# Kernel optimization log

Hardware: AMD Instinct MI355X
Metric: run time of the kernel (lower is better)

Reference implementation:

```python
import jax, jax.numpy as jnp
import numpy as np

D = 1024      # hidden_size
F = 4096      # intermediate_size
E = 16        # num_experts
TOPK = 2      # num_experts_per_tok
B, L = 1, 2048


def setup_inputs() -> dict:
    key = jax.random.key(0)
    ks = jax.random.split(key, 5)
    s = 0.02
    return {
        "x": jax.random.normal(ks[0], (B, L, D), dtype=jnp.float32),
        "gate_w": jax.random.normal(ks[1], (E, D), dtype=jnp.float32) * s,
        "w1s": jax.random.normal(ks[2], (E, F, D), dtype=jnp.float32) * s,  # per-expert w1 (out,in)
        "w2s": jax.random.normal(ks[3], (E, D, F), dtype=jnp.float32) * s,  # per-expert w2
        "w3s": jax.random.normal(ks[4], (E, F, D), dtype=jnp.float32) * s,  # per-expert w3
    }


def reference(x, gate_w, w1s, w2s, w3s):
    b, l, d = x.shape
    xf = x.reshape(-1, d)                                   # [T, D]
    router_logits = xf @ gate_w.T                           # [T, E]
    topw, topi = jax.lax.top_k(router_logits.astype(jnp.float32), TOPK)
    topw = jax.nn.softmax(topw, axis=-1).astype(x.dtype)    # [T, K]
    T = xf.shape[0]
    # dense combine weights: zero for unselected experts (same math as masked loop)
    combine = jnp.zeros((T, E), x.dtype).at[jnp.arange(T)[:, None], topi].add(topw)

    def body(acc, ew):
        w1, w2, w3, cw = ew                                 # cw: [T]
        h = jax.nn.silu(xf @ w1.T) * (xf @ w3.T)            # [T, F]
        return acc + cw[:, None] * (h @ w2.T), None

    out, _ = jax.lax.scan(body, jnp.zeros_like(xf), (w1s, w2s, w3s, combine.T))
    return out.reshape(b, l, d), router_logits
```

## Files before the change

### kernel.cpp

```cpp
#include <hip/hip_runtime.h>

#define D_DIM 1024
#define F_DIM 4096
#define E_NUM 16
#define T_NUM 2048

typedef __bf16 bf16x8 __attribute__((ext_vector_type(8)));
typedef float f32x4 __attribute__((ext_vector_type(4)));

__device__ __forceinline__ unsigned pack2bf(float a, float b) {
  unsigned ua = __builtin_bit_cast(unsigned, a);
  unsigned ub = __builtin_bit_cast(unsigned, b);
  return ((ub + 0x8000u) & 0xffff0000u) | ((ua + 0x8000u) >> 16);
}
__device__ __forceinline__ unsigned short f2bf(float a) {
  unsigned ua = __builtin_bit_cast(unsigned, a);
  return (unsigned short)((ua + 0x8000u) >> 16);
}
__device__ __forceinline__ bf16x8 cvt8(f32x4 a, f32x4 b) {
  bf16x8 r;
  r[0] = (__bf16)a[0]; r[1] = (__bf16)a[1]; r[2] = (__bf16)a[2]; r[3] = (__bf16)a[3];
  r[4] = (__bf16)b[0]; r[5] = (__bf16)b[1]; r[6] = (__bf16)b[2]; r[7] = (__bf16)b[3];
  return r;
}
__device__ __forceinline__ void gload16(const void* g, void* l) {
  __builtin_amdgcn_global_load_lds(
      (const __attribute__((address_space(1))) unsigned*)g,
      (__attribute__((address_space(3))) unsigned*)l, 16, 0, 0);
}

__global__ __launch_bounds__(256) void moe_xcast(
    const float* __restrict__ x, unsigned short* __restrict__ xbf)
{
  int i = blockIdx.x * 256 + threadIdx.x;
  const f32x4* p = (const f32x4*)x + (size_t)i * 2;
  f32x4 a = p[0], b = p[1];
  uint4 o;
  o.x = pack2bf(a[0], a[1]); o.y = pack2bf(a[2], a[3]);
  o.z = pack2bf(b[0], b[1]); o.w = pack2bf(b[2], b[3]);
  ((uint4*)xbf)[i] = o;
}

__global__ __launch_bounds__(256) void moe_router(
    const float* __restrict__ x, const float* __restrict__ gate,
    float* __restrict__ logits_out, int* __restrict__ topi, float* __restrict__ topw)
{
  __shared__ float lg[16][17];
  int tid = threadIdx.x;
  int tbase = blockIdx.x * 16;
  int tt = tid >> 4, e = tid & 15;
  const float4* xr = (const float4*)(x + (size_t)(tbase + tt) * D_DIM);
  const float4* gw = (const float4*)(gate + (size_t)e * D_DIM);
  float acc = 0.f;
  #pragma unroll 4
  for (int k = 0; k < D_DIM / 4; ++k) {
    float4 a = xr[k], b = gw[k];
    acc += a.x * b.x + a.y * b.y + a.z * b.z + a.w * b.w;
  }
  lg[tt][e] = acc;
  logits_out[(size_t)(tbase + tt) * E_NUM + e] = acc;
  __syncthreads();
  if (tid < 16) {
    int t = tid;
    float best = -1e30f; int i0 = 0;
    #pragma unroll
    for (int j = 0; j < 16; ++j) { float v = lg[t][j]; if (v > best) { best = v; i0 = j; } }
    float best1 = -1e30f; int i1 = 0;
    #pragma unroll
    for (int j = 0; j < 16; ++j) { if (j == i0) continue; float v = lg[t][j]; if (v > best1) { best1 = v; i1 = j; } }
    float e1 = __expf(best1 - best);
    float inv = 1.f / (1.f + e1);
    int gt = tbase + t;
    topi[gt * 2]     = i0;  topi[gt * 2 + 1] = i1;
    topw[gt * 2]     = inv; topw[gt * 2 + 1] = e1 * inv;
  }
}

__global__ __launch_bounds__(1024) void moe_route_build(
    const int* __restrict__ topi,
    int* __restrict__ cnt, int* __restrict__ rowbase,
    int* __restrict__ rowlist, int* __restrict__ rowpos)
{
  __shared__ int scnt[16];
  __shared__ int sbase[17];
  int wave = threadIdx.x >> 6;
  int lane = threadIdx.x & 63;
  int total = 0;
  for (int c = 0; c < (T_NUM * 2) / 64; ++c) {
    int s = c * 64 + lane;
    unsigned long long m = __ballot(topi[s] == wave);
    total += __popcll(m);
  }
  if (lane == 0) scnt[wave] = total;
  __syncthreads();
  if (threadIdx.x == 0) {
    int acc = 0;
    for (int e2 = 0; e2 < 16; ++e2) { sbase[e2] = acc; cnt[e2] = scnt[e2]; acc += scnt[e2]; }
    sbase[16] = acc;
    for (int e2 = 0; e2 <= 16; ++e2) rowbase[e2] = sbase[e2];
  }
  __syncthreads();
  int running = sbase[wave];
  for (int c = 0; c < (T_NUM * 2) / 64; ++c) {
    int s = c * 64 + lane;
    int ei = topi[s];
    unsigned long long m = __ballot(ei == wave);
    if (ei == wave) {
      int pos = running + __popcll(m & ((1ull << lane) - 1ull));
      rowlist[pos] = s;
      rowpos[s] = pos;
    }
    running += __popcll(m);
  }
}

__global__ __launch_bounds__(512, 2) void moe_gemm1(
    const unsigned short* __restrict__ xbf, const float* __restrict__ w1s, const float* __restrict__ w3s,
    const int* __restrict__ cnt, const int* __restrict__ rowbase, const int* __restrict__ rowlist,
    unsigned short* __restrict__ H)
{
  int bid = blockIdx.x;
  int xcd = bid & 7, j = bid >> 3;
  int e = xcd * 2 + (j >> 5);
  int nt = j & 31;
  int Ne = cnt[e];
  int rbase = rowbase[e];
  int nmt = (Ne + 255) >> 8;

  __shared__ char smem[98304];

  int tid = threadIdx.x, lane = tid & 63, wave = tid >> 6;

  const float* w1e = w1s + (size_t)e * F_DIM * D_DIM + (size_t)(nt * 128) * D_DIM;
  const float* w3e = w3s + (size_t)e * F_DIM * D_DIM + (size_t)(nt * 128) * D_DIM;
  const char* p1[2]; const char* p3[2];
  #pragma unroll
  for (int it = 0; it < 2; ++it) {
    int r = (wave * 2 + it) * 8 + (lane >> 3);
    int c = (lane & 7) ^ (r & 7);
    p1[it] = (const char*)(w1e + (size_t)r * D_DIM) + c * 16;
    p3[it] = (const char*)(w3e + (size_t)r * D_DIM) + c * 16;
  }

  int xrr[2]; int xc[2];
  #pragma unroll
  for (int it = 0; it < 2; ++it) {
    xrr[it] = (wave * 2 + it) * 16 + (lane >> 2);
    xc[it] = (lane & 3) ^ ((xrr[it] >> 1) & 3);
  }

  int wm = wave >> 1, wn = wave & 1;
  int lr16 = lane & 15, lq = lane >> 4;

  unsigned offA[4];
  #pragma unroll
  for (int mi = 0; mi < 4; ++mi) {
    int m = wm * 64 + mi * 16 + lr16;
    offA[mi] = (unsigned)(m * 64 + ((lq ^ ((m >> 1) & 3)) * 16));
  }
  unsigned offB[4][2];
  #pragma unroll
  for (int ni = 0; ni < 4; ++ni) {
    int n = wn * 64 + ni * 16 + lr16;
    #pragma unroll
    for (int h = 0; h < 2; ++h)
      offB[ni][h] = (unsigned)(n * 128 + (((lq * 2 + h) ^ (n & 7)) * 16));
  }

  unsigned xdst = (unsigned)((wave * 2) * 1024 + lane * 16);
  unsigned wdst = (unsigned)((wave * 2) * 1024 + lane * 16);

  for (int mt = 0; mt < nmt; ++mt) {
    const char* px[2];
    #pragma unroll
    for (int it = 0; it < 2; ++it) {
      int xlr = mt * 256 + xrr[it];
      int tok = (xlr < Ne) ? (rowlist[rbase + xlr] >> 1) : 0;
      px[it] = (const char*)(xbf + (size_t)tok * D_DIM) + xc[it] * 16;
    }

    f32x4 acc1[4][4], acc3[4][4];
    #pragma unroll
    for (int i = 0; i < 4; ++i)
      #pragma unroll
      for (int jj = 0; jj < 4; ++jj) { acc1[i][jj] = {0.f,0.f,0.f,0.f}; acc3[i][jj] = {0.f,0.f,0.f,0.f}; }

    auto STAGE = [&](unsigned bsel, int ks) {
      gload16(px[0] + ks * 64, smem + bsel * 16384 + xdst);
      gload16(px[1] + ks * 64, smem + bsel * 16384 + xdst + 1024);
      #pragma unroll
      for (int it = 0; it < 2; ++it) {
        gload16(p1[it] + ks * 128, smem + 32768 + bsel * 16384 + wdst + it * 1024);
        gload16(p3[it] + ks * 128, smem + 65536 + bsel * 16384 + wdst + it * 1024);
      }
    };

    STAGE(0, 0);
    unsigned buf = 0;
    for (int ks = 0; ks < 32; ++ks) {
      if (ks < 31) {
        STAGE(buf ^ 1u, ks + 1);
        asm volatile("s_waitcnt vmcnt(6)" ::: "memory");
      } else {
        asm volatile("s_waitcnt vmcnt(0)" ::: "memory");
      }
      __builtin_amdgcn_s_barrier();
      unsigned xb = buf * 16384;
      unsigned w1b = 32768 + buf * 16384;
      unsigned w3b = 65536 + buf * 16384;
      bf16x8 af[4];
      #pragma unroll
      for (int mi = 0; mi < 4; ++mi)
        af[mi] = *(const bf16x8*)(smem + xb + offA[mi]);
      #pragma unroll
      for (int ni = 0; ni < 4; ++ni) {
        bf16x8 b1 = cvt8(*(const f32x4*)(smem + w1b + offB[ni][0]),
                         *(const f32x4*)(smem + w1b + offB[ni][1]));
        bf16x8 b3 = cvt8(*(const f32x4*)(smem + w3b + offB[ni][0]),
                         *(const f32x4*)(smem + w3b + offB[ni][1]));
        #pragma unroll
        for (int mi = 0; mi < 4; ++mi) {
          acc1[mi][ni] = __builtin_amdgcn_mfma_f32_16x16x32_bf16(af[mi], b1, acc1[mi][ni], 0, 0, 0);
          acc3[mi][ni] = __builtin_amdgcn_mfma_f32_16x16x32_bf16(af[mi], b3, acc3[mi][ni], 0, 0, 0);
        }
      }
      __builtin_amdgcn_s_barrier();
      buf ^= 1u;
    }

    #pragma unroll
    for (int mi = 0; mi < 4; ++mi) {
      int mb = wm * 64 + mi * 16 + lq * 4;
      #pragma unroll
      for (int r = 0; r < 4; ++r) {
        int lrow = mt * 256 + mb + r;
        if (lrow < Ne) {
          size_t hrow = (size_t)(rbase + lrow) * F_DIM;
          #pragma unroll
          for (int ni = 0; ni < 4; ++ni) {
            int f = nt * 128 + wn * 64 + ni * 16 + lr16;
            float a1v = acc1[mi][ni][r];
            float a3v = acc3[mi][ni][r];
            float hv = (a1v / (1.f + __expf(-a1v))) * a3v;
            H[hrow + f] = f2bf(hv);
          }
        }
      }
    }
  }
}

__global__ __launch_bounds__(512, 2) void moe_gemm2(
    const unsigned short* __restrict__ H, const float* __restrict__ w2s,
    const int* __restrict__ cnt, const int* __restrict__ rowbase,
    unsigned short* __restrict__ Ybf)
{
  int bid = blockIdx.x;
  int xcd = bid & 7, j = bid >> 3;
  int e = xcd * 2 + (j >> 4);
  int nt = j & 15;
  int Ne = cnt[e];
  int rbase = rowbase[e];
  int nmt = (Ne + 255) >> 8;

  __shared__ char smem[98304];

  int tid = threadIdx.x, lane = tid & 63, wave = tid >> 6;

  const float* w2e = w2s + (size_t)e * D_DIM * F_DIM + (size_t)(nt * 64) * F_DIM;
  const char* pb[2];
  #pragma unroll
  for (int it = 0; it < 2; ++it) {
    int r = (wave * 2 + it) * 4 + (lane >> 4);
    int c = (lane & 15) ^ (r & 7);
    pb[it] = (const char*)(w2e + (size_t)r * F_DIM) + c * 16;
  }

  int arr[4]; int ac[4];
  #pragma unroll
  for (int it = 0; it < 4; ++it) {
    arr[it] = (wave * 4 + it) * 8 + (lane >> 3);
    ac[it] = (lane & 7) ^ (arr[it] & 7);
  }

  int wm = wave >> 1, wn = wave & 1;
  int lr16 = lane & 15, lq = lane >> 4;

  unsigned dst2 = (unsigned)((wave * 2) * 1024 + lane * 16);
  unsigned dst4 = (unsigned)((wave * 4) * 1024 + lane * 16);

  for (int mt = 0; mt < nmt; ++mt) {
    const char* pa[4];
    #pragma unroll
    for (int it = 0; it < 4; ++it) {
      int grow = mt * 256 + arr[it]; if (grow >= Ne) grow = Ne - 1;
      pa[it] = (const char*)(H + (size_t)(rbase + grow) * F_DIM) + ac[it] * 16;
    }

    f32x4 acc[4][2];
    #pragma unroll
    for (int i = 0; i < 4; ++i) { acc[i][0] = {0.f,0.f,0.f,0.f}; acc[i][1] = {0.f,0.f,0.f,0.f}; }

    auto STAGE = [&](unsigned bsel, int ks) {
      #pragma unroll
      for (int it = 0; it < 4; ++it)
        gload16(pa[it] + ks * 128, smem + bsel * 32768 + dst4 + it * 1024);
      #pragma unroll
      for (int it = 0; it < 2; ++it)
        gload16(pb[it] + ks * 256, smem + 65536 + bsel * 16384 + dst2 + it * 1024);
    };

    STAGE(0, 0);
    unsigned buf = 0;
    for (int ks = 0; ks < 64; ++ks) {
      if (ks < 63) {
        STAGE(buf ^ 1u, ks + 1);
        asm volatile("s_waitcnt vmcnt(6)" ::: "memory");
      } else {
        asm volatile("s_waitcnt vmcnt(0)" ::: "memory");
      }
      __builtin_amdgcn_s_barrier();
      unsigned ab = buf * 32768;
      unsigned bb = 65536 + buf * 16384;
      #pragma unroll
      for (int ksub = 0; ksub < 2; ++ksub) {
        bf16x8 bfr[2];
        #pragma unroll
        for (int ni = 0; ni < 2; ++ni) {
          int n = wn * 32 + ni * 16 + lr16;
          unsigned o0 = (unsigned)(n * 256 + (((ksub * 8 + lq * 2 + 0) ^ (n & 7)) * 16));
          unsigned o1 = (unsigned)(n * 256 + (((ksub * 8 + lq * 2 + 1) ^ (n & 7)) * 16));
          bfr[ni] = cvt8(*(const f32x4*)(smem + bb + o0), *(const f32x4*)(smem + bb + o1));
        }
        #pragma unroll
        for (int mi = 0; mi < 4; ++mi) {
          int m = wm * 64 + mi * 16 + lr16;
          unsigned off = (unsigned)(m * 128 + (((ksub * 4 + lq) ^ (m & 7)) * 16));
          bf16x8 af = *(const bf16x8*)(smem + ab + off);
          #pragma unroll
          for (int ni = 0; ni < 2; ++ni)
            acc[mi][ni] = __builtin_amdgcn_mfma_f32_16x16x32_bf16(af, bfr[ni], acc[mi][ni], 0, 0, 0);
        }
      }
      __builtin_amdgcn_s_barrier();
      buf ^= 1u;
    }

    #pragma unroll
    for (int mi = 0; mi < 4; ++mi) {
      int mb = wm * 64 + mi * 16 + lq * 4;
      #pragma unroll
      for (int r = 0; r < 4; ++r) {
        int lrow = mt * 256 + mb + r;
        if (lrow < Ne) {
          size_t yrow = (size_t)(rbase + lrow) * D_DIM;
          #pragma unroll
          for (int ni = 0; ni < 2; ++ni) {
            int d = nt * 64 + wn * 32 + ni * 16 + lr16;
            Ybf[yrow + d] = f2bf(acc[mi][ni][r]);
          }
        }
      }
    }
  }
}

__global__ __launch_bounds__(128) void moe_combine(
    const unsigned short* __restrict__ Ybf, const int* __restrict__ rowpos,
    const float* __restrict__ topw, float* __restrict__ out)
{
  int t = blockIdx.x, tid = threadIdx.x;
  int r0 = rowpos[t * 2], r1 = rowpos[t * 2 + 1];
  float p0 = topw[t * 2], p1 = topw[t * 2 + 1];
  uint4 a = ((const uint4*)(Ybf + (size_t)r0 * D_DIM))[tid];
  uint4 b = ((const uint4*)(Ybf + (size_t)r1 * D_DIM))[tid];
  float4 o0, o1;
  #define LO(u) __builtin_bit_cast(float, (unsigned)((u) << 16))
  #define HI(u) __builtin_bit_cast(float, (unsigned)((u) & 0xffff0000u))
  o0.x = p0 * LO(a.x) + p1 * LO(b.x);  o0.y = p0 * HI(a.x) + p1 * HI(b.x);
  o0.z = p0 * LO(a.y) + p1 * LO(b.y);  o0.w = p0 * HI(a.y) + p1 * HI(b.y);
  o1.x = p0 * LO(a.z) + p1 * LO(b.z);  o1.y = p0 * HI(a.z) + p1 * HI(b.z);
  o1.z = p0 * LO(a.w) + p1 * LO(b.w);  o1.w = p0 * HI(a.w) + p1 * HI(b.w);
  #undef LO
  #undef HI
  float4* orow = (float4*)(out + (size_t)t * D_DIM);
  orow[tid * 2]     = o0;
  orow[tid * 2 + 1] = o1;
}

extern "C" void kernel_launch(void* const* d_in, const int* in_sizes, int n_in,
                              void* d_out, int out_size, void* d_ws, size_t ws_size,
                              hipStream_t stream) {
  const float* x    = (const float*)d_in[0];
  const float* gate = (const float*)d_in[1];
  const float* w1   = (const float*)d_in[2];
  const float* w2   = (const float*)d_in[3];
  const float* w3   = (const float*)d_in[4];
  float* out    = (float*)d_out;
  float* logits = out + (size_t)T_NUM * D_DIM;

  char* ws = (char*)d_ws;
  int*   cnt     = (int*)(ws + 0);
  int*   rowbase = (int*)(ws + 64);
  int*   topi    = (int*)(ws + 1024);
  float* topw    = (float*)(ws + 1024 + 16384);
  int*   rowlist = (int*)(ws + 1024 + 32768);
  int*   rowpos  = (int*)(ws + 1024 + 49152);
  unsigned short* H   = (unsigned short*)(ws + 131072);
  unsigned short* Ybf = (unsigned short*)(ws + 131072 + 33554432);
  unsigned short* xbf = (unsigned short*)(ws + 131072 + 33554432 + 8388608);

  moe_xcast<<<(T_NUM * D_DIM) / (256 * 8), 256, 0, stream>>>(x, xbf);
  moe_router<<<T_NUM / 16, 256, 0, stream>>>(x, gate, logits, topi, topw);
  moe_route_build<<<1, 1024, 0, stream>>>(topi, cnt, rowbase, rowlist, rowpos);
  moe_gemm1<<<512, 512, 0, stream>>>(xbf, w1, w3, cnt, rowbase, rowlist, H);
  moe_gemm2<<<256, 512, 0, stream>>>(H, w2, cnt, rowbase, Ybf);
  moe_combine<<<T_NUM, 128, 0, stream>>>(Ybf, rowpos, topw, out);
}
```

Before: 381.4 us.

## Triple-buffer LDS staging with prefetch distance two in both MoE GEMMs

Both expert GEMM kernels move from double-buffered to triple-buffered shared-memory staging. Tile loads are now issued two k-steps ahead, and the vmcnt waits are adjusted so more global loads stay in flight during the MFMA work. The goal is to hide global memory latency better on the fp32 weight streams. The cost is a larger LDS footprint, rising from 96KB to 144KB per block.

```diff
diff --git a/kernel.cpp b/kernel.cpp
--- a/kernel.cpp
+++ b/kernel.cpp
@@ -127,7 +127,7 @@
   int rbase = rowbase[e];
   int nmt = (Ne + 255) >> 8;
 
-  __shared__ char smem[98304];
+  __shared__ char smem[147456];
 
   int tid = threadIdx.x, lane = tid & 63, wave = tid >> 6;
 
@@ -186,38 +186,41 @@
       for (int jj = 0; jj < 4; ++jj) { acc1[i][jj] = {0.f,0.f,0.f,0.f}; acc3[i][jj] = {0.f,0.f,0.f,0.f}; }
 
     auto STAGE = [&](unsigned bsel, int ks) {
-      gload16(px[0] + ks * 64, smem + bsel * 16384 + xdst);
-      gload16(px[1] + ks * 64, smem + bsel * 16384 + xdst + 1024);
+      unsigned bo = bsel * 16384u;
+      gload16(px[0] + ks * 64, smem + bo + xdst);
+      gload16(px[1] + ks * 64, smem + bo + xdst + 1024);
       #pragma unroll
       for (int it = 0; it < 2; ++it) {
-        gload16(p1[it] + ks * 128, smem + 32768 + bsel * 16384 + wdst + it * 1024);
-        gload16(p3[it] + ks * 128, smem + 65536 + bsel * 16384 + wdst + it * 1024);
+        gload16(p1[it] + ks * 128, smem + 49152 + bo + wdst + it * 1024);
+        gload16(p3[it] + ks * 128, smem + 98304 + bo + wdst + it * 1024);
       }
     };
 
     STAGE(0, 0);
-    unsigned buf = 0;
+    STAGE(1, 1);
+    unsigned cb = 0;
     for (int ks = 0; ks < 32; ++ks) {
-      if (ks < 31) {
-        STAGE(buf ^ 1u, ks + 1);
+      if (ks < 30) {
+        unsigned sb = (cb == 0) ? 2u : cb - 1u;
+        STAGE(sb, ks + 2);
+        asm volatile("s_waitcnt vmcnt(12)" ::: "memory");
+      } else if (ks == 30) {
         asm volatile("s_waitcnt vmcnt(6)" ::: "memory");
       } else {
         asm volatile("s_waitcnt vmcnt(0)" ::: "memory");
       }
       __builtin_amdgcn_s_barrier();
-      unsigned xb = buf * 16384;
-      unsigned w1b = 32768 + buf * 16384;
-      unsigned w3b = 65536 + buf * 16384;
+      unsigned bo = cb * 16384u;
       bf16x8 af[4];
       #pragma unroll
       for (int mi = 0; mi < 4; ++mi)
-        af[mi] = *(const bf16x8*)(smem + xb + offA[mi]);
+        af[mi] = *(const bf16x8*)(smem + bo + offA[mi]);
       #pragma unroll
       for (int ni = 0; ni < 4; ++ni) {
-        bf16x8 b1 = cvt8(*(const f32x4*)(smem + w1b + offB[ni][0]),
-                         *(const f32x4*)(smem + w1b + offB[ni][1]));
-        bf16x8 b3 = cvt8(*(const f32x4*)(smem + w3b + offB[ni][0]),
-                         *(const f32x4*)(smem + w3b + offB[ni][1]));
+        bf16x8 b1 = cvt8(*(const f32x4*)(smem + 49152 + bo + offB[ni][0]),
+                         *(const f32x4*)(smem + 49152 + bo + offB[ni][1]));
+        bf16x8 b3 = cvt8(*(const f32x4*)(smem + 98304 + bo + offB[ni][0]),
+                         *(const f32x4*)(smem + 98304 + bo + offB[ni][1]));
         #pragma unroll
         for (int mi = 0; mi < 4; ++mi) {
           acc1[mi][ni] = __builtin_amdgcn_mfma_f32_16x16x32_bf16(af[mi], b1, acc1[mi][ni], 0, 0, 0);
@@ -225,7 +228,7 @@
         }
       }
       __builtin_amdgcn_s_barrier();
-      buf ^= 1u;
+      cb = (cb == 2) ? 0u : cb + 1u;
     }
 
     #pragma unroll
@@ -263,7 +266,7 @@
   int rbase = rowbase[e];
   int nmt = (Ne + 255) >> 8;
 
-  __shared__ char smem[98304];
+  __shared__ char smem[147456];
 
   int tid = threadIdx.x, lane = tid & 63, wave = tid >> 6;
 
@@ -304,24 +307,28 @@
     auto STAGE = [&](unsigned bsel, int ks) {
       #pragma unroll
       for (int it = 0; it < 4; ++it)
-        gload16(pa[it] + ks * 128, smem + bsel * 32768 + dst4 + it * 1024);
+        gload16(pa[it] + ks * 128, smem + bsel * 32768u + dst4 + it * 1024);
       #pragma unroll
       for (int it = 0; it < 2; ++it)
-        gload16(pb[it] + ks * 256, smem + 65536 + bsel * 16384 + dst2 + it * 1024);
+        gload16(pb[it] + ks * 256, smem + 98304 + bsel * 16384u + dst2 + it * 1024);
     };
 
     STAGE(0, 0);
-    unsigned buf = 0;
+    STAGE(1, 1);
+    unsigned cb = 0;
     for (int ks = 0; ks < 64; ++ks) {
-      if (ks < 63) {
-        STAGE(buf ^ 1u, ks + 1);
+      if (ks < 62) {
+        unsigned sb = (cb == 0) ? 2u : cb - 1u;
+        STAGE(sb, ks + 2);
+        asm volatile("s_waitcnt vmcnt(12)" ::: "memory");
+      } else if (ks == 62) {
         asm volatile("s_waitcnt vmcnt(6)" ::: "memory");
       } else {
         asm volatile("s_waitcnt vmcnt(0)" ::: "memory");
       }
       __builtin_amdgcn_s_barrier();
-      unsigned ab = buf * 32768;
-      unsigned bb = 65536 + buf * 16384;
+      unsigned ab = cb * 32768u;
+      unsigned bb = 98304 + cb * 16384u;
       #pragma unroll
       for (int ksub = 0; ksub < 2; ++ksub) {
         bf16x8 bfr[2];
@@ -343,7 +350,7 @@
         }
       }
       __builtin_amdgcn_s_barrier();
-      buf ^= 1u;
+      cb = (cb == 2) ? 0u : cb + 1u;
     }
 
     #pragma unroll
```

After: 392.4 us. 1.03x slower.

## Split MoE GEMMs over M-tiles in a 3D grid with 320-row tiles

Applied to the files above, without the earlier changes.

Both expert GEMM kernels drop their in-block loop over 256-row M tiles. Each block now handles one 320-row tile, launched over a (N-tile, M-tile, expert) grid, and blocks past the expert's row count exit early. This spreads imbalanced expert loads across more blocks and uses larger M tiles for more weight reuse per loaded tile. In exchange it uses more LDS and accumulator registers per block, which may lower occupancy, drops the XCD-aware expert mapping, and reloads weights once per M tile.

```diff
diff --git a/kernel.cpp b/kernel.cpp
--- a/kernel.cpp
+++ b/kernel.cpp
@@ -119,15 +119,12 @@
     const int* __restrict__ cnt, const int* __restrict__ rowbase, const int* __restrict__ rowlist,
     unsigned short* __restrict__ H)
 {
-  int bid = blockIdx.x;
-  int xcd = bid & 7, j = bid >> 3;
-  int e = xcd * 2 + (j >> 5);
-  int nt = j & 31;
+  int nt = blockIdx.x, mt = blockIdx.y, e = blockIdx.z;
   int Ne = cnt[e];
+  if (mt * 320 >= Ne) return;
   int rbase = rowbase[e];
-  int nmt = (Ne + 255) >> 8;
-
-  __shared__ char smem[98304];
+
+  __shared__ char smem[107520];
 
   int tid = threadIdx.x, lane = tid & 63, wave = tid >> 6;
 
@@ -142,20 +139,31 @@
     p3[it] = (const char*)(w3e + (size_t)r * D_DIM) + c * 16;
   }
 
-  int xrr[2]; int xc[2];
-  #pragma unroll
-  for (int it = 0; it < 2; ++it) {
-    xrr[it] = (wave * 2 + it) * 16 + (lane >> 2);
-    xc[it] = (lane & 3) ^ ((xrr[it] >> 1) & 3);
+  const char* px[3];
+  unsigned xdoff[3];
+  #pragma unroll
+  for (int it = 0; it < 3; ++it) {
+    int ch = wave + it * 8;
+    if (ch < 20) {
+      int r = ch * 16 + (lane >> 2);
+      int lr = mt * 320 + r;
+      int tok = (lr < Ne) ? (rowlist[rbase + lr] >> 1) : 0;
+      int c = (lane & 3) ^ ((r >> 1) & 3);
+      px[it] = (const char*)(xbf + (size_t)tok * D_DIM) + c * 16;
+      xdoff[it] = (unsigned)(ch * 1024 + lane * 16);
+    } else {
+      px[it] = (const char*)xbf + (lane & 3) * 16;
+      xdoff[it] = 0xFFFFFFFFu;
+    }
   }
 
   int wm = wave >> 1, wn = wave & 1;
   int lr16 = lane & 15, lq = lane >> 4;
 
-  unsigned offA[4];
-  #pragma unroll
-  for (int mi = 0; mi < 4; ++mi) {
-    int m = wm * 64 + mi * 16 + lr16;
+  unsigned offA[5];
+  #pragma unroll
+  for (int mi = 0; mi < 5; ++mi) {
+    int m = wm * 80 + mi * 16 + lr16;
     offA[mi] = (unsigned)(m * 64 + ((lq ^ ((m >> 1) & 3)) * 16));
   }
   unsigned offB[4][2];
@@ -167,83 +175,77 @@
       offB[ni][h] = (unsigned)(n * 128 + (((lq * 2 + h) ^ (n & 7)) * 16));
   }
 
-  unsigned xdst = (unsigned)((wave * 2) * 1024 + lane * 16);
   unsigned wdst = (unsigned)((wave * 2) * 1024 + lane * 16);
 
-  for (int mt = 0; mt < nmt; ++mt) {
-    const char* px[2];
+  f32x4 acc1[5][4], acc3[5][4];
+  #pragma unroll
+  for (int i = 0; i < 5; ++i)
+    #pragma unroll
+    for (int j = 0; j < 4; ++j) { acc1[i][j] = {0.f,0.f,0.f,0.f}; acc3[i][j] = {0.f,0.f,0.f,0.f}; }
+
+  auto STAGE = [&](unsigned bsel, int ks) {
+    #pragma unroll
+    for (int it = 0; it < 3; ++it) {
+      char* dst = (xdoff[it] == 0xFFFFFFFFu)
+                    ? (smem + 106496 + lane * 16)
+                    : (smem + bsel * 20480u + xdoff[it]);
+      gload16(px[it] + ks * 64, dst);
+    }
     #pragma unroll
     for (int it = 0; it < 2; ++it) {
-      int xlr = mt * 256 + xrr[it];
-      int tok = (xlr < Ne) ? (rowlist[rbase + xlr] >> 1) : 0;
-      px[it] = (const char*)(xbf + (size_t)tok * D_DIM) + xc[it] * 16;
-    }
-
-    f32x4 acc1[4][4], acc3[4][4];
-    #pragma unroll
-    for (int i = 0; i < 4; ++i)
+      gload16(p1[it] + ks * 128, smem + 40960 + bsel * 16384u + wdst + it * 1024);
+      gload16(p3[it] + ks * 128, smem + 73728 + bsel * 16384u + wdst + it * 1024);
+    }
+  };
+
+  STAGE(0, 0);
+  unsigned buf = 0;
+  for (int ks = 0; ks < 32; ++ks) {
+    if (ks < 31) {
+      STAGE(buf ^ 1u, ks + 1);
+      asm volatile("s_waitcnt vmcnt(7)" ::: "memory");
+    } else {
+      asm volatile("s_waitcnt vmcnt(0)" ::: "memory");
+    }
+    __builtin_amdgcn_s_barrier();
+    unsigned xb = buf * 20480u;
+    unsigned w1b = 40960 + buf * 16384u;
+    unsigned w3b = 73728 + buf * 16384u;
+    bf16x8 af[5];
+    #pragma unroll
+    for (int mi = 0; mi < 5; ++mi)
+      af[mi] = *(const bf16x8*)(smem + xb + offA[mi]);
+    #pragma unroll
+    for (int ni = 0; ni < 4; ++ni) {
+      bf16x8 b1 = cvt8(*(const f32x4*)(smem + w1b + offB[ni][0]),
+                       *(const f32x4*)(smem + w1b + offB[ni][1]));
+      bf16x8 b3 = cvt8(*(const f32x4*)(smem + w3b + offB[ni][0]),
+                       *(const f32x4*)(smem + w3b + offB[ni][1]));
       #pragma unroll
-      for (int jj = 0; jj < 4; ++jj) { acc1[i][jj] = {0.f,0.f,0.f,0.f}; acc3[i][jj] = {0.f,0.f,0.f,0.f}; }
-
-    auto STAGE = [&](unsigned bsel, int ks) {
-      gload16(px[0] + ks * 64, smem + bsel * 16384 + xdst);
-      gload16(px[1] + ks * 64, smem + bsel * 16384 + xdst + 1024);
-      #pragma unroll
-      for (int it = 0; it < 2; ++it) {
-        gload16(p1[it] + ks * 128, smem + 32768 + bsel * 16384 + wdst + it * 1024);
-        gload16(p3[it] + ks * 128, smem + 65536 + bsel * 16384 + wdst + it * 1024);
+      for (int mi = 0; mi < 5; ++mi) {
+        acc1[mi][ni] = __builtin_amdgcn_mfma_f32_16x16x32_bf16(af[mi], b1, acc1[mi][ni], 0, 0, 0);
+        acc3[mi][ni] = __builtin_amdgcn_mfma_f32_16x16x32_bf16(af[mi], b3, acc3[mi][ni], 0, 0, 0);
       }
-    };
-
-    STAGE(0, 0);
-    unsigned buf = 0;
-    for (int ks = 0; ks < 32; ++ks) {
-      if (ks < 31) {
-        STAGE(buf ^ 1u, ks + 1);
-        asm volatile("s_waitcnt vmcnt(6)" ::: "memory");
-      } else {
-        asm volatile("s_waitcnt vmcnt(0)" ::: "memory");
-      }
-      __builtin_amdgcn_s_barrier();
-      unsigned xb = buf * 16384;
-      unsigned w1b = 32768 + buf * 16384;
-      unsigned w3b = 65536 + buf * 16384;
-      bf16x8 af[4];
-      #pragma unroll
-      for (int mi = 0; mi < 4; ++mi)
-        af[mi] = *(const bf16x8*)(smem + xb + offA[mi]);
-      #pragma unroll
-      for (int ni = 0; ni < 4; ++ni) {
-        bf16x8 b1 = cvt8(*(const f32x4*)(smem + w1b + offB[ni][0]),
-                         *(const f32x4*)(smem + w1b + offB[ni][1]));
-        bf16x8 b3 = cvt8(*(const f32x4*)(smem + w3b + offB[ni][0]),
-                         *(const f32x4*)(smem + w3b + offB[ni][1]));
+    }
+    __builtin_amdgcn_s_barrier();
+    buf ^= 1u;
+  }
+
+  #pragma unroll
+  for (int mi = 0; mi < 5; ++mi) {
+    int mb = wm * 80 + mi * 16 + lq * 4;
+    #pragma unroll
+    for (int r = 0; r < 4; ++r) {
+      int lrow = mt * 320 + mb + r;
+      if (lrow < Ne) {
+        size_t hrow = (size_t)(rbase + lrow) * F_DIM;
         #pragma unroll
-        for (int mi = 0; mi < 4; ++mi) {
-          acc1[mi][ni] = __builtin_amdgcn_mfma_f32_16x16x32_bf16(af[mi], b1, acc1[mi][ni], 0, 0, 0);
-          acc3[mi][ni] = __builtin_amdgcn_mfma_f32_16x16x32_bf16(af[mi], b3, acc3[mi][ni], 0, 0, 0);
-        }
-      }
-      __builtin_amdgcn_s_barrier();
-      buf ^= 1u;
-    }
-
-    #pragma unroll
-    for (int mi = 0; mi < 4; ++mi) {
-      int mb = wm * 64 + mi * 16 + lq * 4;
-      #pragma unroll
-      for (int r = 0; r < 4; ++r) {
-        int lrow = mt * 256 + mb + r;
-        if (lrow < Ne) {
-          size_t hrow = (size_t)(rbase + lrow) * F_DIM;
-          #pragma unroll
-          for (int ni = 0; ni < 4; ++ni) {
-            int f = nt * 128 + wn * 64 + ni * 16 + lr16;
-            float a1v = acc1[mi][ni][r];
-            float a3v = acc3[mi][ni][r];
-            float hv = (a1v / (1.f + __expf(-a1v))) * a3v;
-            H[hrow + f] = f2bf(hv);
-          }
+        for (int ni = 0; ni < 4; ++ni) {
+          int f = nt * 128 + wn * 64 + ni * 16 + lr16;
+          float a1v = acc1[mi][ni][r];
+          float a3v = acc3[mi][ni][r];
+          float hv = (a1v / (1.f + __expf(-a1v))) * a3v;
+          H[hrow + f] = f2bf(hv);
         }
       }
     }
@@ -255,15 +257,12 @@
     const int* __restrict__ cnt, const int* __restrict__ rowbase,
     unsigned short* __restrict__ Ybf)
 {
-  int bid = blockIdx.x;
-  int xcd = bid & 7, j = bid >> 3;
-  int e = xcd * 2 + (j >> 4);
-  int nt = j & 15;
+  int nt = blockIdx.x, mt = blockIdx.y, e = blockIdx.z;
   int Ne = cnt[e];
+  if (mt * 320 >= Ne) return;
   int rbase = rowbase[e];
-  int nmt = (Ne + 255) >> 8;
-
-  __shared__ char smem[98304];
+
+  __shared__ char smem[114688];
 
   int tid = threadIdx.x, lane = tid & 63, wave = tid >> 6;
 
@@ -276,89 +275,84 @@
     pb[it] = (const char*)(w2e + (size_t)r * F_DIM) + c * 16;
   }
 
-  int arr[4]; int ac[4];
-  #pragma unroll
-  for (int it = 0; it < 4; ++it) {
-    arr[it] = (wave * 4 + it) * 8 + (lane >> 3);
-    ac[it] = (lane & 7) ^ (arr[it] & 7);
+  const char* pa[5];
+  unsigned adoff[5];
+  #pragma unroll
+  for (int it = 0; it < 5; ++it) {
+    int ch = wave + it * 8;
+    int r = ch * 8 + (lane >> 3);
+    int grow = mt * 320 + r; if (grow >= Ne) grow = Ne - 1;
+    int c = (lane & 7) ^ (r & 7);
+    pa[it] = (const char*)(H + (size_t)(rbase + grow) * F_DIM) + c * 16;
+    adoff[it] = (unsigned)(ch * 1024 + lane * 16);
   }
 
   int wm = wave >> 1, wn = wave & 1;
   int lr16 = lane & 15, lq = lane >> 4;
 
-  unsigned dst2 = (unsigned)((wave * 2) * 1024 + lane * 16);
-  unsigned dst4 = (unsigned)((wave * 4) * 1024 + lane * 16);
-
-  for (int mt = 0; mt < nmt; ++mt) {
-    const char* pa[4];
-    #pragma unroll
-    for (int it = 0; it < 4; ++it) {
-      int grow = mt * 256 + arr[it]; if (grow >= Ne) grow = Ne - 1;
-      pa[it] = (const char*)(H + (size_t)(rbase + grow) * F_DIM) + ac[it] * 16;
-    }
-
-    f32x4 acc[4][2];
-    #pragma unroll
-    for (int i = 0; i < 4; ++i) { acc[i][0] = {0.f,0.f,0.f,0.f}; acc[i][1] = {0.f,0.f,0.f,0.f}; }
-
-    auto STAGE = [&](unsigned bsel, int ks) {
+  unsigned dstB = (unsigned)((wave * 2) * 1024 + lane * 16);
+
+  f32x4 acc[5][2];
+  #pragma unroll
+  for (int i = 0; i < 5; ++i) { acc[i][0] = {0.f,0.f,0.f,0.f}; acc[i][1] = {0.f,0.f,0.f,0.f}; }
+
+  auto STAGE = [&](unsigned bsel, int ks) {
+    #pragma unroll
+    for (int it = 0; it < 5; ++it)
+      gload16(pa[it] + ks * 128, smem + bsel * 40960u + adoff[it]);
+    #pragma unroll
+    for (int it = 0; it < 2; ++it)
+      gload16(pb[it] + ks * 256, smem + 81920 + bsel * 16384u + dstB + it * 1024);
+  };
+
+  STAGE(0, 0);
+  unsigned buf = 0;
+  for (int ks = 0; ks < 64; ++ks) {
+    if (ks < 63) {
+      STAGE(buf ^ 1u, ks + 1);
+      asm volatile("s_waitcnt vmcnt(7)" ::: "memory");
+    } else {
+      asm volatile("s_waitcnt vmcnt(0)" ::: "memory");
+    }
+    __builtin_amdgcn_s_barrier();
+    unsigned ab = buf * 40960u;
+    unsigned bb = 81920 + buf * 16384u;
+    #pragma unroll
+    for (int ksub = 0; ksub < 2; ++ksub) {
+      bf16x8 bfr[2];
       #pragma unroll
-      for (int it = 0; it < 4; ++it)
-        gload16(pa[it] + ks * 128, smem + bsel * 32768 + dst4 + it * 1024);
+      for (int ni = 0; ni < 2; ++ni) {
+        int n = wn * 32 + ni * 16 + lr16;
+        unsigned o0 = (unsigned)(n * 256 + (((ksub * 8 + lq * 2 + 0) ^ (n & 7)) * 16));
+        unsigned o1 = (unsigned)(n * 256 + (((ksub * 8 + lq * 2 + 1) ^ (n & 7)) * 16));
+        bfr[ni] = cvt8(*(const f32x4*)(smem + bb + o0), *(const f32x4*)(smem + bb + o1));
+      }
       #pragma unroll
-      for (int it = 0; it < 2; ++it)
-        gload16(pb[it] + ks * 256, smem + 65536 + bsel * 16384 + dst2 + it * 1024);
-    };
-
-    STAGE(0, 0);
-    unsigned buf = 0;
-    for (int ks = 0; ks < 64; ++ks) {
-      if (ks < 63) {
-        STAGE(buf ^ 1u, ks + 1);
-        asm volatile("s_waitcnt vmcnt(6)" ::: "memory");
-      } else {
-        asm volatile("s_waitcnt vmcnt(0)" ::: "memory");
+      for (int mi = 0; mi < 5; ++mi) {
+        int m = wm * 80 + mi * 16 + lr16;
+        unsigned off = (unsigned)(m * 128 + (((ksub * 4 + lq) ^ (m & 7)) * 16));
+        bf16x8 af = *(const bf16x8*)(smem + ab + off);
+        #pragma unroll
+        for (int ni = 0; ni < 2; ++ni)
+          acc[mi][ni] = __builtin_amdgcn_mfma_f32_16x16x32_bf16(af, bfr[ni], acc[mi][ni], 0, 0, 0);
       }
-      __builtin_amdgcn_s_barrier();
-      unsigned ab = buf * 32768;
-      unsigned bb = 65536 + buf * 16384;
-      #pragma unroll
-      for (int ksub = 0; ksub < 2; ++ksub) {
-        bf16x8 bfr[2];
+    }
+    __builtin_amdgcn_s_barrier();
+    buf ^= 1u;
+  }
+
+  #pragma unroll
+  for (int mi = 0; mi < 5; ++mi) {
+    int mb = wm * 80 + mi * 16 + lq * 4;
+    #pragma unroll
+    for (int r = 0; r < 4; ++r) {
+      int lrow = mt * 320 + mb + r;
+      if (lrow < Ne) {
+        size_t yrow = (size_t)(rbase + lrow) * D_DIM;
         #pragma unroll
         for (int ni = 0; ni < 2; ++ni) {
-          int n = wn * 32 + ni * 16 + lr16;
-          unsigned o0 = (unsigned)(n * 256 + (((ksub * 8 + lq * 2 + 0) ^ (n & 7)) * 16));
-          unsigned o1 = (unsigned)(n * 256 + (((ksub * 8 + lq * 2 + 1) ^ (n & 7)) * 16));
-          bfr[ni] = cvt8(*(const f32x4*)(smem + bb + o0), *(const f32x4*)(smem + bb + o1));
-        }
-        #pragma unroll
-        for (int mi = 0; mi < 4; ++mi) {
-          int m = wm * 64 + mi * 16 + lr16;
-          unsigned off = (unsigned)(m * 128 + (((ksub * 4 + lq) ^ (m & 7)) * 16));
-          bf16x8 af = *(const bf16x8*)(smem + ab + off);
-          #pragma unroll
-          for (int ni = 0; ni < 2; ++ni)
-            acc[mi][ni] = __builtin_amdgcn_mfma_f32_16x16x32_bf16(af, bfr[ni], acc[mi][ni], 0, 0, 0);
-        }
-      }
-      __builtin_amdgcn_s_barrier();
-      buf ^= 1u;
-    }
-
-    #pragma unroll
-    for (int mi = 0; mi < 4; ++mi) {
-      int mb = wm * 64 + mi * 16 + lq * 4;
-      #pragma unroll
-      for (int r = 0; r < 4; ++r) {
-        int lrow = mt * 256 + mb + r;
-        if (lrow < Ne) {
-          size_t yrow = (size_t)(rbase + lrow) * D_DIM;
-          #pragma unroll
-          for (int ni = 0; ni < 2; ++ni) {
-            int d = nt * 64 + wn * 32 + ni * 16 + lr16;
-            Ybf[yrow + d] = f2bf(acc[mi][ni][r]);
-          }
+          int d = nt * 64 + wn * 32 + ni * 16 + lr16;
+          Ybf[yrow + d] = f2bf(acc[mi][ni][r]);
         }
       }
     }
@@ -413,7 +407,7 @@
   moe_xcast<<<(T_NUM * D_DIM) / (256 * 8), 256, 0, stream>>>(x, xbf);
   moe_router<<<T_NUM / 16, 256, 0, stream>>>(x, gate, logits, topi, topw);
   moe_route_build<<<1, 1024, 0, stream>>>(topi, cnt, rowbase, rowlist, rowpos);
-  moe_gemm1<<<512, 512, 0, stream>>>(xbf, w1, w3, cnt, rowbase, rowlist, H);
-  moe_gemm2<<<256, 512, 0, stream>>>(H, w2, cnt, rowbase, Ybf);
+  moe_gemm1<<<dim3(32, 4, 16), 512, 0, stream>>>(xbf, w1, w3, cnt, rowbase, rowlist, H);
+  moe_gemm2<<<dim3(16, 4, 16), 512, 0, stream>>>(H, w2, cnt, rowbase, Ybf);
   moe_combine<<<T_NUM, 128, 0, stream>>>(Ybf, rowpos, topw, out);
 }
```

Result: faster. 344.4 us (-9.7%).
